# Kernel tuning notes

Measured on AMD Instinct MI355X. Metric: run time of the kernel, lower is better.

## Reference

```python
import jax, jax.numpy as jnp
import numpy as np

N_NODES = 200000
N_SUPER = 20000
N_EDGES = 640000
EMB = 256


def setup_inputs() -> dict:
    key = jax.random.key(0)
    ks = jax.random.split(key, 8)
    x = jax.random.normal(ks[0], (N_NODES, EMB), dtype=jnp.float32)
    new_supernode_x = jax.random.normal(ks[1], (N_SUPER, EMB), dtype=jnp.float32)
    supernode_edge_index = jax.random.randint(ks[2], (2, N_EDGES), 0, N_NODES, dtype=jnp.int64)
    # supernode indices must be unique (torch `x[idx] += v` assumes no duplicate writes)
    supernode_idx = jnp.arange(N_SUPER, dtype=jnp.int64)
    graph_batch = jax.random.randint(ks[3], (N_NODES,), 0, 1024, dtype=jnp.int64)  # unused by forward
    s = 1.0 / np.sqrt(EMB)  # torch.nn.Linear default init scale
    W1 = jax.random.uniform(ks[4], (EMB, EMB), minval=-s, maxval=s, dtype=jnp.float32)
    b1 = jax.random.uniform(ks[5], (EMB,), minval=-s, maxval=s, dtype=jnp.float32)
    W2 = jax.random.uniform(ks[6], (EMB, EMB), minval=-s, maxval=s, dtype=jnp.float32)
    b2 = jax.random.uniform(ks[7], (EMB,), minval=-s, maxval=s, dtype=jnp.float32)
    return {
        "x": x,
        "new_supernode_x": new_supernode_x,
        "supernode_edge_index": supernode_edge_index,
        "supernode_idx": supernode_idx,
        "graph_batch": graph_batch,
        "W1": W1,
        "b1": b1,
        "W2": W2,
        "b2": b2,
    }


def reference(x, new_supernode_x, supernode_edge_index, supernode_idx, graph_batch, W1, b1, W2, b2):
    # step 1: project metagraph supernode embeddings, add into bg-graph rows at supernode_idx
    sn_proj = new_supernode_x @ W1.T + b1                 # [S, D]
    x1 = x.at[supernode_idx].add(sn_proj)                 # [N, D]
    # step 2: gather src rows (AFTER step-1 update), project, scatter-add to dst rows
    src = supernode_edge_index[1]
    dst = supernode_edge_index[0]
    msg = x1[src] @ W2.T + b2                             # [E, D]
    return x1.at[dst].add(msg)                            # [N, D]
```

## Files before the change

kernel.cpp:

```cpp
#include <hip/hip_runtime.h>

#define N_NODES 200000
#define N_SUPER 20000
#define N_EDGES 640000
#define EMB 256

typedef unsigned short ushort_t;
typedef __attribute__((ext_vector_type(8))) short bf16x8;
typedef __attribute__((ext_vector_type(4))) float f32x4;

static __device__ __forceinline__ ushort_t f2bf(float f) {
    unsigned int b = __float_as_uint(f);
    unsigned int r = (b + 0x7FFFu + ((b >> 16) & 1u)) >> 16;
    return (ushort_t)r;
}

__global__ __launch_bounds__(256) void copy_f4(const float4* __restrict__ s,
                                               float4* __restrict__ d, int n) {
    int i = blockIdx.x * 256 + threadIdx.x;
    if (i < n) d[i] = s[i];
}

__global__ __launch_bounds__(256) void hist_dst(const int* __restrict__ ei,
                                                int* __restrict__ counts) {
    int e = blockIdx.x * 256 + threadIdx.x;
    if (e < N_EDGES) atomicAdd(&counts[ei[e]], 1);
}

__global__ __launch_bounds__(256) void block_sums(const int* __restrict__ counts,
                                                  int* __restrict__ partials, int N) {
    __shared__ int sh[256];
    int tid = threadIdx.x;
    int i = blockIdx.x * 256 + tid;
    sh[tid] = (i < N) ? counts[i] : 0;
    __syncthreads();
    for (int off = 128; off > 0; off >>= 1) {
        if (tid < off) sh[tid] += sh[tid + off];
        __syncthreads();
    }
    if (tid == 0) partials[blockIdx.x] = sh[0];
}

__global__ __launch_bounds__(256) void scan_partials(int* __restrict__ partials, int NB) {
    __shared__ int sh[256];
    int tid = threadIdx.x;
    int carry = 0;
    for (int c0 = 0; c0 < NB; c0 += 256) {
        int i = c0 + tid;
        int v = (i < NB) ? partials[i] : 0;
        sh[tid] = v;
        __syncthreads();
        for (int off = 1; off < 256; off <<= 1) {
            int t = (tid >= off) ? sh[tid - off] : 0;
            __syncthreads();
            sh[tid] += t;
            __syncthreads();
        }
        int incl = sh[tid];
        int total = sh[255];
        if (i < NB) partials[i] = carry + incl - v;
        carry += total;
        __syncthreads();
    }
}

__global__ __launch_bounds__(256) void scan_blocks(const int* __restrict__ counts,
                                                   const int* __restrict__ partials,
                                                   int* __restrict__ base, int N) {
    __shared__ int sh[256];
    int tid = threadIdx.x;
    int b = blockIdx.x;
    int i = b * 256 + tid;
    int c = (i < N) ? counts[i] : 0;
    sh[tid] = c;
    __syncthreads();
    for (int off = 1; off < 256; off <<= 1) {
        int t = (tid >= off) ? sh[tid - off] : 0;
        __syncthreads();
        sh[tid] += t;
        __syncthreads();
    }
    if (i < N) base[i] = partials[b] + sh[tid] - c;
    if (i == N - 1) base[N] = partials[b] + sh[tid];
}

__global__ __launch_bounds__(256) void fill_bucket(const int* __restrict__ ei,
                                                   const int* __restrict__ base,
                                                   int* __restrict__ cursor,
                                                   int* __restrict__ bucket) {
    int e = blockIdx.x * 256 + threadIdx.x;
    if (e >= N_EDGES) return;
    int d = ei[e];
    int s = ei[N_EDGES + e];
    int pos = atomicAdd(&cursor[d], 1);
    bucket[base[d] + pos] = s;
}

__global__ __launch_bounds__(256) void gather_sum(const int* __restrict__ bucket,
                                                  const int* __restrict__ base,
                                                  const float* __restrict__ x1,
                                                  ushort_t* __restrict__ agg) {
    int node = blockIdx.x * 4 + (threadIdx.x >> 6);
    int lane = threadIdx.x & 63;
    if (node >= N_NODES) return;
    int j0 = base[node], j1 = base[node + 1];
    float4 acc = make_float4(0.f, 0.f, 0.f, 0.f);
    for (int j = j0; j < j1; ++j) {
        int s = bucket[j];
        float4 v = *(const float4*)(x1 + (size_t)s * EMB + lane * 4);
        acc.x += v.x; acc.y += v.y; acc.z += v.z; acc.w += v.w;
    }
    ushort4 p;
    p.x = f2bf(acc.x); p.y = f2bf(acc.y); p.z = f2bf(acc.z); p.w = f2bf(acc.w);
    *(ushort4*)(agg + (size_t)node * EMB + lane * 4) = p;
}

template <bool A_BF16>
__global__ __launch_bounds__(512) void gemm_mfma(
    const void* __restrict__ Ap, const float* __restrict__ W,
    const float* __restrict__ bias, const int* __restrict__ deg,
    const int* __restrict__ idx, float* __restrict__ out,
    int M, int ntiles) {
    const int lane = threadIdx.x & 63;
    const int wave = threadIdx.x >> 6;
    const int col0 = wave * 32;
    const int lcol = lane & 15;
    const int lk8  = (lane >> 4) * 8;

    bf16x8 bh[2][8], bl[2][8];
    #pragma unroll
    for (int nt = 0; nt < 2; ++nt) {
        const float* wr = W + (size_t)(col0 + nt * 16 + lcol) * EMB + lk8;
        #pragma unroll
        for (int kk = 0; kk < 8; ++kk) {
            float4 u0 = *(const float4*)(wr + kk * 32);
            float4 u1 = *(const float4*)(wr + kk * 32 + 4);
            float uv[8] = {u0.x, u0.y, u0.z, u0.w, u1.x, u1.y, u1.z, u1.w};
            bf16x8 h, l;
            #pragma unroll
            for (int j = 0; j < 8; ++j) {
                ushort_t hb = f2bf(uv[j]);
                h[j] = (short)hb;
                float hf = __uint_as_float((unsigned int)hb << 16);
                l[j] = (short)f2bf(uv[j] - hf);
            }
            bh[nt][kk] = h;
            bl[nt][kk] = l;
        }
    }
    float bias_v[2];
    #pragma unroll
    for (int nt = 0; nt < 2; ++nt) bias_v[nt] = bias[col0 + nt * 16 + lcol];

    for (int tile = blockIdx.x; tile < ntiles; tile += gridDim.x) {
        const int row0 = tile * 16;
        f32x4 acc[2] = {{0.f, 0.f, 0.f, 0.f}, {0.f, 0.f, 0.f, 0.f}};

        if constexpr (A_BF16) {
            const ushort_t* A0 = (const ushort_t*)Ap + (size_t)(row0 + lcol) * EMB + lk8;
            #pragma unroll
            for (int kk = 0; kk < 8; ++kk) {
                bf16x8 a = *(const bf16x8*)(A0 + kk * 32);
                #pragma unroll
                for (int nt = 0; nt < 2; ++nt) {
                    acc[nt] = __builtin_amdgcn_mfma_f32_16x16x32_bf16(a, bh[nt][kk], acc[nt], 0, 0, 0);
                    acc[nt] = __builtin_amdgcn_mfma_f32_16x16x32_bf16(a, bl[nt][kk], acc[nt], 0, 0, 0);
                }
            }
        } else {
            const float* A0 = (const float*)Ap + (size_t)(row0 + lcol) * EMB + lk8;
            #pragma unroll
            for (int kk = 0; kk < 8; ++kk) {
                float4 a0 = *(const float4*)(A0 + kk * 32);
                float4 a1 = *(const float4*)(A0 + kk * 32 + 4);
                float av[8] = {a0.x, a0.y, a0.z, a0.w, a1.x, a1.y, a1.z, a1.w};
                bf16x8 ah, al;
                #pragma unroll
                for (int j = 0; j < 8; ++j) {
                    ushort_t hb = f2bf(av[j]);
                    ah[j] = (short)hb;
                    float hf = __uint_as_float((unsigned int)hb << 16);
                    al[j] = (short)f2bf(av[j] - hf);
                }
                #pragma unroll
                for (int nt = 0; nt < 2; ++nt) {
                    acc[nt] = __builtin_amdgcn_mfma_f32_16x16x32_bf16(ah, bh[nt][kk], acc[nt], 0, 0, 0);
                    acc[nt] = __builtin_amdgcn_mfma_f32_16x16x32_bf16(al, bh[nt][kk], acc[nt], 0, 0, 0);
                    acc[nt] = __builtin_amdgcn_mfma_f32_16x16x32_bf16(ah, bl[nt][kk], acc[nt], 0, 0, 0);
                }
            }
        }

        #pragma unroll
        for (int j = 0; j < 4; ++j) {
            const int r = row0 + (lane >> 4) * 4 + j;
            const int orow = idx ? idx[r] : r;
            const float coef = deg ? (float)deg[r] : 1.0f;
            float* op = out + (size_t)orow * EMB + col0 + lcol;
            #pragma unroll
            for (int nt = 0; nt < 2; ++nt)
                op[nt * 16] += acc[nt][j] + bias_v[nt] * coef;
        }
    }
}

extern "C" void kernel_launch(void* const* d_in, const int* in_sizes, int n_in,
                              void* d_out, int out_size, void* d_ws, size_t ws_size,
                              hipStream_t stream) {
    const float* x    = (const float*)d_in[0];
    const float* snx  = (const float*)d_in[1];
    const int*   ei   = (const int*)d_in[2];
    const int*   sidx = (const int*)d_in[3];
    const float* W1   = (const float*)d_in[5];
    const float* b1   = (const float*)d_in[6];
    const float* W2   = (const float*)d_in[7];
    const float* b2   = (const float*)d_in[8];
    float* out = (float*)d_out;

    ushort_t* agg  = (ushort_t*)d_ws;
    int* counts    = (int*)(agg + (size_t)N_NODES * EMB);
    int* cursor    = counts + N_NODES;
    int* base      = cursor + N_NODES;
    int* bucket    = base + (N_NODES + 1);
    int* partials  = bucket + N_EDGES;

    const int NB = (N_NODES + 255) / 256;

    hipMemsetAsync(counts, 0, 2 * N_NODES * sizeof(int), stream);

    int n4 = N_NODES * EMB / 4;
    copy_f4<<<(n4 + 255) / 256, 256, 0, stream>>>((const float4*)x, (float4*)out, n4);

    gemm_mfma<false><<<512, 512, 0, stream>>>(snx, W1, b1, nullptr, sidx, out,
                                              N_SUPER, N_SUPER / 16);

    hist_dst<<<(N_EDGES + 255) / 256, 256, 0, stream>>>(ei, counts);
    block_sums<<<NB, 256, 0, stream>>>(counts, partials, N_NODES);
    scan_partials<<<1, 256, 0, stream>>>(partials, NB);
    scan_blocks<<<NB, 256, 0, stream>>>(counts, partials, base, N_NODES);
    fill_bucket<<<(N_EDGES + 255) / 256, 256, 0, stream>>>(ei, base, cursor, bucket);

    gather_sum<<<(N_NODES + 3) / 4, 256, 0, stream>>>(bucket, base, out, agg);

    gemm_mfma<true><<<1024, 512, 0, stream>>>(agg, W2, b2, counts, nullptr, out,
                                              N_NODES, N_NODES / 16);
}
```

Before: 970.1 us.

## Retile MFMA GEMM to 32-row tiles split across two column blocks, unroll gather

The GEMM kernel now gives each wave 16 output columns and 32 rows per tile instead of 32 columns and 16 rows. Column halves are split across a second grid dimension, which halves the per-wave weight registers and raises occupancy with a launch-bounds hint. The old output values are prefetched before the MFMA loop so the read-modify-write latency overlaps with compute. The gather-sum loop is unrolled by four so more independent row loads are in flight, at the cost of a slightly different summation order and each A tile now being read by two blocks.

```diff
diff --git a/kernel.cpp b/kernel.cpp
--- a/kernel.cpp
+++ b/kernel.cpp
@@ -105,10 +105,22 @@
     if (node >= N_NODES) return;
     int j0 = base[node], j1 = base[node + 1];
     float4 acc = make_float4(0.f, 0.f, 0.f, 0.f);
-    for (int j = j0; j < j1; ++j) {
-        int s = bucket[j];
-        float4 v = *(const float4*)(x1 + (size_t)s * EMB + lane * 4);
-        acc.x += v.x; acc.y += v.y; acc.z += v.z; acc.w += v.w;
+    int j = j0;
+    for (; j + 3 < j1; j += 4) {
+        int s0 = bucket[j], s1 = bucket[j + 1], s2 = bucket[j + 2], s3 = bucket[j + 3];
+        float4 v0 = *(const float4*)(x1 + (size_t)s0 * EMB + lane * 4);
+        float4 v1 = *(const float4*)(x1 + (size_t)s1 * EMB + lane * 4);
+        float4 v2 = *(const float4*)(x1 + (size_t)s2 * EMB + lane * 4);
+        float4 v3 = *(const float4*)(x1 + (size_t)s3 * EMB + lane * 4);
+        acc.x += (v0.x + v1.x) + (v2.x + v3.x);
+        acc.y += (v0.y + v1.y) + (v2.y + v3.y);
+        acc.z += (v0.z + v1.z) + (v2.z + v3.z);
+        acc.w += (v0.w + v1.w) + (v2.w + v3.w);
+    }
+    for (; j < j1; ++j) {
+        int s0 = bucket[j];
+        float4 v0 = *(const float4*)(x1 + (size_t)s0 * EMB + lane * 4);
+        acc.x += v0.x; acc.y += v0.y; acc.z += v0.z; acc.w += v0.w;
     }
     ushort4 p;
     p.x = f2bf(acc.x); p.y = f2bf(acc.y); p.z = f2bf(acc.z); p.w = f2bf(acc.w);
@@ -116,21 +128,21 @@
 }
 
 template <bool A_BF16>
-__global__ __launch_bounds__(512) void gemm_mfma(
+__global__ __launch_bounds__(512, 3) void gemm_mfma(
     const void* __restrict__ Ap, const float* __restrict__ W,
     const float* __restrict__ bias, const int* __restrict__ deg,
     const int* __restrict__ idx, float* __restrict__ out,
     int M, int ntiles) {
-    const int lane = threadIdx.x & 63;
-    const int wave = threadIdx.x >> 6;
-    const int col0 = wave * 32;
-    const int lcol = lane & 15;
-    const int lk8  = (lane >> 4) * 8;
-
-    bf16x8 bh[2][8], bl[2][8];
-    #pragma unroll
-    for (int nt = 0; nt < 2; ++nt) {
-        const float* wr = W + (size_t)(col0 + nt * 16 + lcol) * EMB + lk8;
+    const int lane  = threadIdx.x & 63;
+    const int wave  = threadIdx.x >> 6;
+    const int l16   = lane & 15;
+    const int lrow4 = (lane >> 4) * 4;
+    const int lk8   = (lane >> 4) * 8;
+    const int col   = blockIdx.y * 128 + wave * 16 + l16;
+
+    bf16x8 bh[8], bl[8];
+    {
+        const float* wr = W + (size_t)col * EMB + lk8;
         #pragma unroll
         for (int kk = 0; kk < 8; ++kk) {
             float4 u0 = *(const float4*)(wr + kk * 32);
@@ -144,63 +156,81 @@
                 float hf = __uint_as_float((unsigned int)hb << 16);
                 l[j] = (short)f2bf(uv[j] - hf);
             }
-            bh[nt][kk] = h;
-            bl[nt][kk] = l;
+            bh[kk] = h;
+            bl[kk] = l;
         }
     }
-    float bias_v[2];
-    #pragma unroll
-    for (int nt = 0; nt < 2; ++nt) bias_v[nt] = bias[col0 + nt * 16 + lcol];
+    const float bias_v = bias[col];
 
     for (int tile = blockIdx.x; tile < ntiles; tile += gridDim.x) {
-        const int row0 = tile * 16;
+        const int row0 = tile * 32;
+
+        int   orow[2][4];
+        float coef[2][4];
+        float oldv[2][4];
+        #pragma unroll
+        for (int mf = 0; mf < 2; ++mf)
+            #pragma unroll
+            for (int j = 0; j < 4; ++j) {
+                const int r = row0 + mf * 16 + lrow4 + j;
+                const int o = idx ? idx[r] : r;
+                orow[mf][j] = o;
+                coef[mf][j] = deg ? (float)deg[r] : 1.0f;
+                oldv[mf][j] = out[(size_t)o * EMB + col];
+            }
+
         f32x4 acc[2] = {{0.f, 0.f, 0.f, 0.f}, {0.f, 0.f, 0.f, 0.f}};
 
         if constexpr (A_BF16) {
-            const ushort_t* A0 = (const ushort_t*)Ap + (size_t)(row0 + lcol) * EMB + lk8;
+            const ushort_t* Ab = (const ushort_t*)Ap;
+            #pragma unroll
+            for (int h = 0; h < 2; ++h) {
+                bf16x8 a[4][2];
+                #pragma unroll
+                for (int kk = 0; kk < 4; ++kk)
+                    #pragma unroll
+                    for (int mf = 0; mf < 2; ++mf)
+                        a[kk][mf] = *(const bf16x8*)(Ab +
+                            (size_t)(row0 + mf * 16 + l16) * EMB + (h * 4 + kk) * 32 + lk8);
+                #pragma unroll
+                for (int kk = 0; kk < 4; ++kk)
+                    #pragma unroll
+                    for (int mf = 0; mf < 2; ++mf) {
+                        acc[mf] = __builtin_amdgcn_mfma_f32_16x16x32_bf16(a[kk][mf], bh[h * 4 + kk], acc[mf], 0, 0, 0);
+                        acc[mf] = __builtin_amdgcn_mfma_f32_16x16x32_bf16(a[kk][mf], bl[h * 4 + kk], acc[mf], 0, 0, 0);
+                    }
+            }
+        } else {
+            const float* Af = (const float*)Ap;
             #pragma unroll
             for (int kk = 0; kk < 8; ++kk) {
-                bf16x8 a = *(const bf16x8*)(A0 + kk * 32);
                 #pragma unroll
-                for (int nt = 0; nt < 2; ++nt) {
-                    acc[nt] = __builtin_amdgcn_mfma_f32_16x16x32_bf16(a, bh[nt][kk], acc[nt], 0, 0, 0);
-                    acc[nt] = __builtin_amdgcn_mfma_f32_16x16x32_bf16(a, bl[nt][kk], acc[nt], 0, 0, 0);
+                for (int mf = 0; mf < 2; ++mf) {
+                    const float* ar = Af + (size_t)(row0 + mf * 16 + l16) * EMB + kk * 32 + lk8;
+                    float4 a0 = *(const float4*)ar;
+                    float4 a1 = *(const float4*)(ar + 4);
+                    float av[8] = {a0.x, a0.y, a0.z, a0.w, a1.x, a1.y, a1.z, a1.w};
+                    bf16x8 ah, al;
+                    #pragma unroll
+                    for (int j = 0; j < 8; ++j) {
+                        ushort_t hb = f2bf(av[j]);
+                        ah[j] = (short)hb;
+                        float hf = __uint_as_float((unsigned int)hb << 16);
+                        al[j] = (short)f2bf(av[j] - hf);
+                    }
+                    acc[mf] = __builtin_amdgcn_mfma_f32_16x16x32_bf16(ah, bh[kk], acc[mf], 0, 0, 0);
+                    acc[mf] = __builtin_amdgcn_mfma_f32_16x16x32_bf16(al, bh[kk], acc[mf], 0, 0, 0);
+                    acc[mf] = __builtin_amdgcn_mfma_f32_16x16x32_bf16(ah, bl[kk], acc[mf], 0, 0, 0);
                 }
             }
-        } else {
-            const float* A0 = (const float*)Ap + (size_t)(row0 + lcol) * EMB + lk8;
-            #pragma unroll
-            for (int kk = 0; kk < 8; ++kk) {
-                float4 a0 = *(const float4*)(A0 + kk * 32);
-                float4 a1 = *(const float4*)(A0 + kk * 32 + 4);
-                float av[8] = {a0.x, a0.y, a0.z, a0.w, a1.x, a1.y, a1.z, a1.w};
-                bf16x8 ah, al;
-                #pragma unroll
-                for (int j = 0; j < 8; ++j) {
-                    ushort_t hb = f2bf(av[j]);
-                    ah[j] = (short)hb;
-                    float hf = __uint_as_float((unsigned int)hb << 16);
-                    al[j] = (short)f2bf(av[j] - hf);
-                }
-                #pragma unroll
-                for (int nt = 0; nt < 2; ++nt) {
-                    acc[nt] = __builtin_amdgcn_mfma_f32_16x16x32_bf16(ah, bh[nt][kk], acc[nt], 0, 0, 0);
-                    acc[nt] = __builtin_amdgcn_mfma_f32_16x16x32_bf16(al, bh[nt][kk], acc[nt], 0, 0, 0);
-                    acc[nt] = __builtin_amdgcn_mfma_f32_16x16x32_bf16(ah, bl[nt][kk], acc[nt], 0, 0, 0);
-                }
-            }
         }
 
         #pragma unroll
-        for (int j = 0; j < 4; ++j) {
-            const int r = row0 + (lane >> 4) * 4 + j;
-            const int orow = idx ? idx[r] : r;
-            const float coef = deg ? (float)deg[r] : 1.0f;
-            float* op = out + (size_t)orow * EMB + col0 + lcol;
-            #pragma unroll
-            for (int nt = 0; nt < 2; ++nt)
-                op[nt * 16] += acc[nt][j] + bias_v[nt] * coef;
-        }
+        for (int mf = 0; mf < 2; ++mf)
+            #pragma unroll
+            for (int j = 0; j < 4; ++j)
+                out[(size_t)orow[mf][j] * EMB + col] =
+                    oldv[mf][j] + acc[mf][j] + bias_v * coef[mf][j];
     }
 }
 
@@ -231,8 +261,8 @@
     int n4 = N_NODES * EMB / 4;
     copy_f4<<<(n4 + 255) / 256, 256, 0, stream>>>((const float4*)x, (float4*)out, n4);
 
-    gemm_mfma<false><<<512, 512, 0, stream>>>(snx, W1, b1, nullptr, sidx, out,
-                                              N_SUPER, N_SUPER / 16);
+    gemm_mfma<false><<<dim3(N_SUPER / 32, 2), 512, 0, stream>>>(
+        snx, W1, b1, nullptr, sidx, out, N_SUPER, N_SUPER / 32);
 
     hist_dst<<<(N_EDGES + 255) / 256, 256, 0, stream>>>(ei, counts);
     block_sums<<<NB, 256, 0, stream>>>(counts, partials, N_NODES);
@@ -242,6 +272,6 @@
 
     gather_sum<<<(N_NODES + 3) / 4, 256, 0, stream>>>(bucket, base, out, agg);
 
-    gemm_mfma<true><<<1024, 512, 0, stream>>>(agg, W2, b2, counts, nullptr, out,
-                                              N_NODES, N_NODES / 16);
-}
+    gemm_mfma<true><<<dim3(1024, 2), 512, 0, stream>>>(
+        agg, W2, b2, counts, nullptr, out, N_NODES, N_NODES / 32);
+}
```

Result: faster. 935.5 us (-3.6%).
